# Kernel optimization log

Hardware: AMD Instinct MI355X
Metric: run time of the kernel (lower is better)

The kernel has to match this reference:

```python
import jax, jax.numpy as jnp
import numpy as np

DIM = 1024
HEADS = 16
DIM_HEAD = 64
INNER = HEADS * DIM_HEAD  # 1024
SCALE = DIM_HEAD ** -0.5


def setup_inputs() -> dict:
    key = jax.random.key(0)
    ks = jax.random.split(key, 7)
    b, n = 4, 1024
    x = jax.random.normal(ks[0], (b, n, DIM), dtype=jnp.float32)
    # Dense kernels (glorot-ish scale), mix-head matrices are N(0,1) as in source
    Wq = jax.random.normal(ks[1], (DIM, INNER), dtype=jnp.float32) * (DIM ** -0.5)
    Wkv = jax.random.normal(ks[2], (DIM, 2 * INNER), dtype=jnp.float32) * (DIM ** -0.5)
    mix_pre = jax.random.normal(ks[3], (HEADS, HEADS), dtype=jnp.float32)
    mix_post = jax.random.normal(ks[4], (HEADS, HEADS), dtype=jnp.float32)
    Wo = jax.random.normal(ks[5], (INNER, DIM), dtype=jnp.float32) * (INNER ** -0.5)
    bo = jnp.zeros((DIM,), dtype=jnp.float32)
    return {"x": x, "Wq": Wq, "Wkv": Wkv, "mix_pre": mix_pre,
            "mix_post": mix_post, "Wo": Wo, "bo": bo}


def reference(x, Wq, Wkv, mix_pre, mix_post, Wo, bo):
    b, n, _ = x.shape
    # context = x (self-attention path)
    q = x @ Wq                      # [b, n, inner]
    kv = x @ Wkv                    # [b, n, 2*inner]
    k, v = jnp.split(kv, 2, axis=-1)
    split_heads = lambda t: t.reshape(b, n, HEADS, DIM_HEAD).transpose(0, 2, 1, 3)
    q, k, v = map(split_heads, (q, k, v))  # [b, h, n, d]
    dots = jnp.einsum('bhid,bhjd->bhij', q, k) * SCALE
    dots = jnp.einsum('bhij,hg->bgij', dots, mix_pre)   # talking-heads pre-softmax
    attn = jax.nn.softmax(dots, axis=-1)
    attn = jnp.einsum('bhij,hg->bgij', attn, mix_post)  # talking-heads post-softmax
    out = jnp.einsum('bhij,bhjd->bhid', attn, v)        # [b, h, n, d]
    out = out.transpose(0, 2, 1, 3).reshape(b, n, INNER)
    return out @ Wo + bo            # dropout rate 0 -> identity
```

## Files before the change

### kernel.cpp

```cpp
#include <hip/hip_runtime.h>
#include <hip/hip_bf16.h>

using bf16 = __hip_bfloat16;

typedef __bf16 bf16x8 __attribute__((ext_vector_type(8)));
typedef __bf16 bf16x2v __attribute__((ext_vector_type(2)));
typedef float  f32x4  __attribute__((ext_vector_type(4)));
typedef float  f32x16 __attribute__((ext_vector_type(16)));

#define QK_SCALE 0.125f

__device__ __forceinline__ void load_lds16(const bf16* g, bf16* l) {
  __builtin_amdgcn_global_load_lds(
      (const __attribute__((address_space(1))) unsigned int*)g,
      (__attribute__((address_space(3))) unsigned int*)l, 16, 0, 0);
}

__device__ __forceinline__ unsigned pack_bf2(float a, float b) {
  bf16x2v v;
  v[0] = (__bf16)a;
  v[1] = (__bf16)b;
  return __builtin_bit_cast(unsigned, v);
}

struct alignas(8) bf16x4s { bf16 a, b, c, d; };
__global__ void f32_to_bf16_k(const float4* __restrict__ in, bf16x4s* __restrict__ out, int n4)
{
  const int i = blockIdx.x * blockDim.x + threadIdx.x;
  if (i < n4) {
    const float4 v = in[i];
    out[i] = { (bf16)v.x, (bf16)v.y, (bf16)v.z, (bf16)v.w };
  }
}

template<int TM, int TN, int WM, int WN, bool BIAS, typename CT>
__global__ __launch_bounds__(256, 2)
void gemm_nt(const bf16* __restrict__ A, const bf16* __restrict__ B,
             CT* __restrict__ C, const float* __restrict__ bias,
             int K, int lda, int ldb, int ldc,
             long sA0, long sA1, long sB0, long sB1, long sC0, long sC1,
             int nz1, float alpha)
{
  constexpr int BK = 32;
  constexpr int LDE = TN + 8;
  constexpr unsigned SB_STAGE = (TM + TN) * BK * 2;
  constexpr unsigned SB_EP = (sizeof(CT) == 2) ? TM * LDE * 2 : 0;
  constexpr unsigned SBYTES = SB_STAGE > SB_EP ? SB_STAGE : SB_EP;
  __shared__ __align__(16) char smem[SBYTES];
  bf16* lsA = (bf16*)smem;
  bf16* lsB = lsA + TM * BK;

  const int z = blockIdx.z;
  A += (long)(z / nz1) * sA0 + (long)(z % nz1) * sA1;
  B += (long)(z / nz1) * sB0 + (long)(z % nz1) * sB1;
  C += (long)(z / nz1) * sC0 + (long)(z % nz1) * sC1;
  const int tm0 = blockIdx.y * TM;
  const int tn0 = blockIdx.x * TN;

  const int tid = threadIdx.x;
  const int w = tid >> 6, l = tid & 63;
  constexpr int WCOLS = TN / WN;
  const int wm = (w / WCOLS) * WM, wn = (w % WCOLS) * WN;
  constexpr int AM = WM / 16, AN = WN / 16;
  f32x4 acc[AM][AN] = {};
  const int kg = l >> 4, rl = l & 15;

  constexpr int RA = TM / 64, RB = TN / 64;
  const int srow0 = tid >> 2;
  const int scol = tid & 3;

  for (int k0 = 0; k0 < K; k0 += BK) {
#pragma unroll
    for (int r = 0; r < RA; ++r) {
      const int row = r * 64 + srow0;
      const int col8 = scol ^ ((row >> 1) & 3);
      load_lds16(A + (long)(tm0 + row) * lda + (k0 + col8 * 8),
                 &lsA[row * BK + scol * 8]);
    }
#pragma unroll
    for (int r = 0; r < RB; ++r) {
      const int row = r * 64 + srow0;
      const int col8 = scol ^ ((row >> 1) & 3);
      load_lds16(B + (long)(tn0 + row) * ldb + (k0 + col8 * 8),
                 &lsB[row * BK + scol * 8]);
    }
    __syncthreads();

    bf16x8 af[AM], bfr[AN];
#pragma unroll
    for (int i = 0; i < AM; ++i) {
      const int m = wm + i * 16 + rl;
      const int p = kg ^ ((m >> 1) & 3);
      af[i] = *(const bf16x8*)&lsA[m * BK + p * 8];
    }
#pragma unroll
    for (int j = 0; j < AN; ++j) {
      const int n = wn + j * 16 + rl;
      const int p = kg ^ ((n >> 1) & 3);
      bfr[j] = *(const bf16x8*)&lsB[n * BK + p * 8];
    }
#pragma unroll
    for (int i = 0; i < AM; ++i)
#pragma unroll
      for (int j = 0; j < AN; ++j)
        acc[i][j] = __builtin_amdgcn_mfma_f32_16x16x32_bf16(af[i], bfr[j], acc[i][j], 0, 0, 0);
    __syncthreads();
  }

  if constexpr (sizeof(CT) == 2) {
    bf16* ep = (bf16*)smem;
#pragma unroll
    for (int i = 0; i < AM; ++i) {
#pragma unroll
      for (int j = 0; j < AN; ++j) {
        const int col = wn + j * 16 + rl;
        float bv = 0.f;
        if (BIAS) bv = bias[tn0 + col];
#pragma unroll
        for (int v = 0; v < 4; ++v) {
          const int row = wm + i * 16 + (l >> 4) * 4 + v;
          ep[row * LDE + col] = (bf16)(acc[i][j][v] * alpha + bv);
        }
      }
    }
    __syncthreads();
    constexpr int CH = (TM * TN) / 2048;
#pragma unroll
    for (int c = 0; c < CH; ++c) {
      const int gidx = (c * 256 + tid) * 8;
      const int row = gidx / TN, col = gidx % TN;
      *(uint4*)&C[(long)(tm0 + row) * ldc + tn0 + col] = *(const uint4*)&ep[row * LDE + col];
    }
  } else {
#pragma unroll
    for (int i = 0; i < AM; ++i) {
#pragma unroll
      for (int j = 0; j < AN; ++j) {
        const int col = tn0 + wn + j * 16 + rl;
        float bv = 0.f;
        if (BIAS) bv = bias[col];
#pragma unroll
        for (int v = 0; v < 4; ++v) {
          const int row = tm0 + wm + i * 16 + (l >> 4) * 4 + v;
          C[(long)row * ldc + col] = (CT)(acc[i][j][v] * alpha + bv);
        }
      }
    }
  }
}

template<typename TI>
__global__ void transpose_k(const TI* __restrict__ in, bf16* __restrict__ out,
                            int ldi, int ldo,
                            long sI0, long sI1, long sO0, long sO1, int nz1)
{
  __shared__ bf16 t[32][33];
  const int z = blockIdx.z;
  in  += (long)(z / nz1) * sI0 + (long)(z % nz1) * sI1;
  out += (long)(z / nz1) * sO0 + (long)(z % nz1) * sO1;
  const int c0 = blockIdx.x * 32, r0 = blockIdx.y * 32;
  const int x = threadIdx.x, y = threadIdx.y;
#pragma unroll
  for (int dy = 0; dy < 32; dy += 8)
    t[y + dy][x] = (bf16)(float)in[(long)(r0 + y + dy) * ldi + c0 + x];
  __syncthreads();
#pragma unroll
  for (int dy = 0; dy < 32; dy += 8)
    out[(long)(c0 + y + dy) * ldo + r0 + x] = t[x][y + dy];
}

__global__ __launch_bounds__(512, 1)
void mix_pv_fused(const bf16* __restrict__ S, const bf16* __restrict__ VTm,
                  bf16* __restrict__ O,
                  const float* __restrict__ mixpre, const float* __restrict__ mixpost)
{
  constexpr int SH = 1032;
  __shared__ __align__(16) __bf16 Sst[2][16 * SH];
  __shared__ __align__(16) __bf16 Pl[2][16 * 16 * 72];
  __shared__ float preS[256], postS[256];

  const int tid = threadIdx.x;
  const int l = tid & 63, w = tid >> 6;
  const int bx = blockIdx.x;
  const int b = bx & 3;
  const int i0 = (bx >> 2) << 4;

  if (tid < 256) preS[tid] = mixpre[tid];
  else           postS[tid - 256] = mixpost[tid - 256];
  __syncthreads();

  const int col = l & 31;
  const int H = l >> 5;
  const int g16 = l & 15;
  const bool loRow = (l & 16) != 0;
  const int rl16 = l & 15, kg4 = l >> 4;

  bf16x8 aPre, aPost;
#pragma unroll
  for (int e = 0; e < 8; ++e) {
    const int k = H * 8 + e;
    {
      const float c = preS[k * 16 + g16];
      const __bf16 hi = (__bf16)c;
      aPre[e] = loRow ? (__bf16)(c - (float)hi) : hi;
    }
    {
      const float c = postS[k * 16 + g16];
      const __bf16 hi = (__bf16)c;
      aPost[e] = loRow ? (__bf16)(c - (float)hi) : hi;
    }
  }

  const bf16* Sb = S + (long)b * 16777216 + (long)i0 * 1024;

  auto stage = [&](int t, int bufi) {
    const int jt = t * 64;
#pragma unroll
    for (int s = 0; s < 4; ++s) {
      const int h = 2 * w + (s >> 1);
      const int half = s & 1;
      const int i = half * 8 + (l >> 3);
      const int j = (l & 7) * 8;
      load_lds16(Sb + (long)h * 1048576 + (long)i * 1024 + jt + j,
                 (bf16*)&Sst[bufi][h * SH + half * 512 + l * 8]);
    }
  };

  float zac[2][8];
#pragma unroll
  for (int il = 0; il < 2; ++il)
#pragma unroll
    for (int k = 0; k < 8; ++k) zac[il][k] = 0.f;

  stage(0, 0);
  for (int t = 0; t < 16; ++t) {
    __syncthreads();
    if (t < 15) stage(t + 1, (t + 1) & 1);
    const __bf16* sb = Sst[t & 1];
#pragma unroll
    for (int il = 0; il < 2; ++il) {
      const int ic = 2 * w + il;
#pragma unroll
      for (int jh = 0; jh < 2; ++jh) {
        bf16x8 bfr;
#pragma unroll
        for (int e = 0; e < 8; ++e)
          bfr[e] = sb[(H * 8 + e) * SH + ic * 64 + jh * 32 + col];
        f32x16 d = {};
        d = __builtin_amdgcn_mfma_f32_32x32x16_bf16(aPre, bfr, d, 0, 0, 0);
#pragma unroll
        for (int k = 0; k < 8; ++k)
          zac[il][k] += __expf(d[k] + d[k + 8] - 10.f);
      }
    }
  }

#pragma unroll
  for (int il = 0; il < 2; ++il)
#pragma unroll
    for (int k = 0; k < 8; ++k) {
      float z = zac[il][k];
      z += __shfl_xor(z, 1, 64);
      z += __shfl_xor(z, 2, 64);
      z += __shfl_xor(z, 4, 64);
      z += __shfl_xor(z, 8, 64);
      z += __shfl_xor(z, 16, 64);
      zac[il][k] = 1.f / z;
    }

  f32x4 acc[2][4] = {};
  uint4 vreg[16];
  const bf16* vtg0 = VTm + ((long)(b * 16 + w) * 64) * 1024;
  const bf16* vtg1 = VTm + ((long)(b * 16 + w + 8) * 64) * 1024;

  stage(0, 0);
  for (int t = 0; t <= 16; ++t) {
    __syncthreads();

    if (t < 15) stage(t + 1, (t + 1) & 1);

    if (t > 0) {
      const __bf16* pb = Pl[(t - 1) & 1];
#pragma unroll
      for (int gi = 0; gi < 2; ++gi) {
        const int G = w + gi * 8;
#pragma unroll
        for (int kc = 0; kc < 2; ++kc) {
          const bf16x8 af = *(const bf16x8*)&pb[G * 1152 + rl16 * 72 + kc * 32 + kg4 * 8];
#pragma unroll
          for (int dt = 0; dt < 4; ++dt) {
            const bf16x8 bfv = __builtin_bit_cast(bf16x8, vreg[gi * 8 + kc * 4 + dt]);
            acc[gi][dt] = __builtin_amdgcn_mfma_f32_16x16x32_bf16(af, bfv, acc[gi][dt], 0, 0, 0);
          }
        }
      }
    }

    if (t < 16) {
      const int jt = t * 64;
#pragma unroll
      for (int kc = 0; kc < 2; ++kc)
#pragma unroll
        for (int dt = 0; dt < 4; ++dt) {
          vreg[kc * 4 + dt] =
              *(const uint4*)&vtg0[(long)(dt * 16 + rl16) * 1024 + jt + kc * 32 + kg4 * 8];
          vreg[8 + kc * 4 + dt] =
              *(const uint4*)&vtg1[(long)(dt * 16 + rl16) * 1024 + jt + kc * 32 + kg4 * 8];
        }

      const __bf16* sb = Sst[t & 1];
      __bf16* pl = Pl[t & 1];
#pragma unroll
      for (int il = 0; il < 2; ++il) {
        const int ic = 2 * w + il;
#pragma unroll
        for (int jh = 0; jh < 2; ++jh) {
          bf16x8 bfr;
#pragma unroll
          for (int e = 0; e < 8; ++e)
            bfr[e] = sb[(H * 8 + e) * SH + ic * 64 + jh * 32 + col];
          f32x16 d = {};
          d = __builtin_amdgcn_mfma_f32_32x32x16_bf16(aPre, bfr, d, 0, 0, 0);
          float pn[8];
#pragma unroll
          for (int k = 0; k < 8; ++k)
            pn[k] = __expf(d[k] + d[k + 8] - 10.f) * zac[il][k];
          const unsigned pA = pack_bf2(pn[0], pn[1]);
          const unsigned pB = pack_bf2(pn[2], pn[3]);
          const unsigned pC = pack_bf2(pn[4], pn[5]);
          const unsigned pD = pack_bf2(pn[6], pn[7]);
          const unsigned x0 = (unsigned)__shfl_xor((int)(H ? pA : pC), 32, 64);
          const unsigned x1 = (unsigned)__shfl_xor((int)(H ? pB : pD), 32, 64);
          uint4 praw;
          praw.x = H ? x0 : pA;
          praw.y = H ? x1 : pB;
          praw.z = H ? pC : x0;
          praw.w = H ? pD : x1;
          const bf16x8 pfr = __builtin_bit_cast(bf16x8, praw);
          f32x16 d2 = {};
          d2 = __builtin_amdgcn_mfma_f32_32x32x16_bf16(aPost, pfr, d2, 0, 0, 0);
#pragma unroll
          for (int k = 0; k < 8; ++k) {
            const int G = k + (k & 4) + (H << 2);
            pl[G * 1152 + ic * 72 + jh * 32 + col] = (__bf16)(d2[k] + d2[k + 8]);
          }
        }
      }
    }
  }

  const long ob = (long)(b * 1024 + i0) * 1024;
#pragma unroll
  for (int gi = 0; gi < 2; ++gi) {
    const int G = w + gi * 8;
#pragma unroll
    for (int dt = 0; dt < 4; ++dt)
#pragma unroll
      for (int v = 0; v < 4; ++v)
        O[ob + (long)((l >> 4) * 4 + v) * 1024 + G * 64 + dt * 16 + rl16] =
            (bf16)acc[gi][dt][v];
  }
}

extern "C" void kernel_launch(void* const* d_in, const int* in_sizes, int n_in,
                              void* d_out, int out_size, void* d_ws, size_t ws_size,
                              hipStream_t stream)
{
  const float* x     = (const float*)d_in[0];
  const float* Wq    = (const float*)d_in[1];
  const float* Wkv   = (const float*)d_in[2];
  const float* mpre  = (const float*)d_in[3];
  const float* mpost = (const float*)d_in[4];
  const float* Wo    = (const float*)d_in[5];
  const float* bo    = (const float*)d_in[6];
  float* out = (float*)d_out;

  char* ws = (char*)d_ws;
  const size_t MB = 1024 * 1024;
  if (ws_size < 184 * MB) return;
  bf16* xb   = (bf16*)(ws);
  bf16* QKV  = (bf16*)(ws + 8 * MB);
  bf16* WT   = (bf16*)(ws + 32 * MB);
  bf16* WoT  = (bf16*)(ws + 38 * MB);
  bf16* VT   = (bf16*)(ws + 40 * MB);
  bf16* Obuf = (bf16*)(ws + 48 * MB);
  bf16* Sbuf = (bf16*)(ws + 56 * MB);

  const dim3 tb(32, 8, 1);

  f32_to_bf16_k<<<4096, 256, 0, stream>>>((const float4*)x, (bf16x4s*)xb, 1048576);

  transpose_k<float><<<dim3(32, 32, 1), tb, 0, stream>>>(Wq,  WT,           1024, 1024, 0, 0, 0, 0, 1);
  transpose_k<float><<<dim3(64, 32, 1), tb, 0, stream>>>(Wkv, WT + 1048576, 2048, 1024, 0, 0, 0, 0, 1);
  transpose_k<float><<<dim3(32, 32, 1), tb, 0, stream>>>(Wo,  WoT,          1024, 1024, 0, 0, 0, 0, 1);

  gemm_nt<128, 128, 64, 64, false, bf16><<<dim3(24, 32, 1), 256, 0, stream>>>(
      xb, WT, QKV, nullptr, 1024, 1024, 1024, 3072, 0, 0, 0, 0, 0, 0, 1, 1.f);

  transpose_k<bf16><<<dim3(2, 32, 64), tb, 0, stream>>>(
      QKV + 2048, VT, 3072, 1024,
      3145728, 64, 16L * 65536, 65536, 16);

  gemm_nt<128, 128, 64, 64, false, bf16><<<dim3(8, 8, 64), 256, 0, stream>>>(
      QKV, QKV + 1024, Sbuf, nullptr, 64, 3072, 3072, 1024,
      3145728, 64, 3145728, 64, 16L * 1048576, 1048576, 16, QK_SCALE);

  mix_pv_fused<<<dim3(256, 1, 1), 512, 0, stream>>>(Sbuf, VT, Obuf, mpre, mpost);

  gemm_nt<128, 128, 64, 64, true, float><<<dim3(8, 32, 1), 256, 0, stream>>>(
      Obuf, WoT, out, bo, 1024, 1024, 1024, 1024, 0, 0, 0, 0, 0, 0, 1, 1.f);
}
```

Baseline: 291.7 us.

## Store scores head-interleaved and load them straight into registers in mix kernel

A new QK kernel writes the score tensor in a [b,i,j,head] layout, so each lane of the talking-heads mix kernel can fetch its 8-head MFMA operand with a single 16-byte global load. This replaces the LDS staging and the strided 8-element gathers from LDS. The softmax and PV loops now double-buffer score fragments in registers and use one lgkm-wait barrier per step, and the P tile stride is padded. The risks are a less efficient QK GEMM with scattered 8-byte stores, and higher register pressure in the fused kernel.

```diff
diff --git a/kernel.cpp b/kernel.cpp
--- a/kernel.cpp
+++ b/kernel.cpp
@@ -21,6 +21,10 @@
   v[0] = (__bf16)a;
   v[1] = (__bf16)b;
   return __builtin_bit_cast(unsigned, v);
+}
+
+__device__ __forceinline__ void barrier_lgkm() {
+  asm volatile("s_waitcnt lgkmcnt(0)\n\ts_barrier" ::: "memory");
 }
 
 struct alignas(8) bf16x4s { bf16 a, b, c, d; };
@@ -169,14 +173,48 @@
     out[(long)(c0 + y + dy) * ldo + r0 + x] = t[x][y + dy];
 }
 
+__global__ __launch_bounds__(256)
+void qk_int(const bf16* __restrict__ QKV, bf16* __restrict__ Sx)
+{
+  const int tid = threadIdx.x;
+  const int l = tid & 63, w = tid >> 6;
+  const int j0 = blockIdx.x * 32, i0 = blockIdx.y * 32, b = blockIdx.z;
+  const int row = l & 31, H = l >> 5;
+
+  const bf16* qb = QKV + (long)(b * 1024 + i0 + row) * 3072 + H * 8;
+  const bf16* kb = QKV + (long)(b * 1024 + j0 + row) * 3072 + 1024 + H * 8;
+  const int h0 = w * 4;
+
+  f32x16 acc[4] = {};
+#pragma unroll
+  for (int hh = 0; hh < 4; ++hh) {
+    const int hofs = (h0 + hh) * 64;
+#pragma unroll
+    for (int kc = 0; kc < 4; ++kc) {
+      const bf16x8 a  = *(const bf16x8*)(qb + hofs + kc * 16);
+      const bf16x8 bb = *(const bf16x8*)(kb + hofs + kc * 16);
+      acc[hh] = __builtin_amdgcn_mfma_f32_32x32x16_bf16(a, bb, acc[hh], 0, 0, 0);
+    }
+  }
+
+  bf16* sb = Sx + ((long)(b * 1024 + i0) * 1024 + j0) * 16 + h0;
+#pragma unroll
+  for (int k = 0; k < 16; ++k) {
+    const int irow = (k & 3) + 8 * (k >> 2) + 4 * H;
+    uint2 pv;
+    pv.x = pack_bf2(acc[0][k] * QK_SCALE, acc[1][k] * QK_SCALE);
+    pv.y = pack_bf2(acc[2][k] * QK_SCALE, acc[3][k] * QK_SCALE);
+    *(uint2*)(sb + (long)irow * 16384 + row * 16) = pv;
+  }
+}
+
 __global__ __launch_bounds__(512, 1)
 void mix_pv_fused(const bf16* __restrict__ S, const bf16* __restrict__ VTm,
                   bf16* __restrict__ O,
                   const float* __restrict__ mixpre, const float* __restrict__ mixpost)
 {
-  constexpr int SH = 1032;
-  __shared__ __align__(16) __bf16 Sst[2][16 * SH];
-  __shared__ __align__(16) __bf16 Pl[2][16 * 16 * 72];
+  constexpr int PLG = 1160;
+  __shared__ __align__(16) __bf16 Pl[2][16 * PLG];
   __shared__ float preS[256], postS[256];
 
   const int tid = threadIdx.x;
@@ -211,19 +249,21 @@
     }
   }
 
-  const bf16* Sb = S + (long)b * 16777216 + (long)i0 * 1024;
-
-  auto stage = [&](int t, int bufi) {
-    const int jt = t * 64;
-#pragma unroll
-    for (int s = 0; s < 4; ++s) {
-      const int h = 2 * w + (s >> 1);
-      const int half = s & 1;
-      const int i = half * 8 + (l >> 3);
-      const int j = (l & 7) * 8;
-      load_lds16(Sb + (long)h * 1048576 + (long)i * 1024 + jt + j,
-                 (bf16*)&Sst[bufi][h * SH + half * 512 + l * 8]);
-    }
+  const bf16* Sb = S + (long)(b * 1024 + i0) * 16384;
+  const bf16* sptr[2][2];
+#pragma unroll
+  for (int il = 0; il < 2; ++il)
+#pragma unroll
+    for (int jh = 0; jh < 2; ++jh)
+      sptr[il][jh] = Sb + (long)(2 * w + il) * 16384 + (jh * 32 + col) * 16 + H * 8;
+
+  auto loadS = [&](uint4* f, int t) {
+    const long to = (long)t * 1024;
+#pragma unroll
+    for (int il = 0; il < 2; ++il)
+#pragma unroll
+      for (int jh = 0; jh < 2; ++jh)
+        f[il * 2 + jh] = *(const uint4*)(sptr[il][jh] + to);
   };
 
   float zac[2][8];
@@ -232,27 +272,28 @@
 #pragma unroll
     for (int k = 0; k < 8; ++k) zac[il][k] = 0.f;
 
-  stage(0, 0);
-  for (int t = 0; t < 16; ++t) {
-    __syncthreads();
-    if (t < 15) stage(t + 1, (t + 1) & 1);
-    const __bf16* sb = Sst[t & 1];
-#pragma unroll
-    for (int il = 0; il < 2; ++il) {
-      const int ic = 2 * w + il;
+  auto mixZ = [&](const uint4* f) {
+#pragma unroll
+    for (int il = 0; il < 2; ++il)
 #pragma unroll
       for (int jh = 0; jh < 2; ++jh) {
-        bf16x8 bfr;
-#pragma unroll
-        for (int e = 0; e < 8; ++e)
-          bfr[e] = sb[(H * 8 + e) * SH + ic * 64 + jh * 32 + col];
+        const bf16x8 bfr = __builtin_bit_cast(bf16x8, f[il * 2 + jh]);
         f32x16 d = {};
         d = __builtin_amdgcn_mfma_f32_32x32x16_bf16(aPre, bfr, d, 0, 0, 0);
 #pragma unroll
         for (int k = 0; k < 8; ++k)
           zac[il][k] += __expf(d[k] + d[k + 8] - 10.f);
       }
-    }
+  };
+
+  uint4 sfA[4], sfB[4];
+
+  loadS(sfA, 0);
+  for (int tt = 0; tt < 16; tt += 2) {
+    loadS(sfB, tt + 1);
+    mixZ(sfA);
+    if (tt + 2 < 16) loadS(sfA, tt + 2);
+    mixZ(sfB);
   }
 
 #pragma unroll
@@ -273,20 +314,48 @@
   const bf16* vtg0 = VTm + ((long)(b * 16 + w) * 64) * 1024;
   const bf16* vtg1 = VTm + ((long)(b * 16 + w + 8) * 64) * 1024;
 
-  stage(0, 0);
-  for (int t = 0; t <= 16; ++t) {
-    __syncthreads();
-
-    if (t < 15) stage(t + 1, (t + 1) & 1);
-
+  auto body = [&](int t, uint4* fcur, uint4* fnext, __bf16* plw, const __bf16* plr) {
+    if (t + 1 < 16) loadS(fnext, t + 1);
+#pragma unroll
+    for (int il = 0; il < 2; ++il) {
+      const int ic = 2 * w + il;
+#pragma unroll
+      for (int jh = 0; jh < 2; ++jh) {
+        const bf16x8 bfr = __builtin_bit_cast(bf16x8, fcur[il * 2 + jh]);
+        f32x16 d = {};
+        d = __builtin_amdgcn_mfma_f32_32x32x16_bf16(aPre, bfr, d, 0, 0, 0);
+        float pn[8];
+#pragma unroll
+        for (int k = 0; k < 8; ++k)
+          pn[k] = __expf(d[k] + d[k + 8] - 10.f) * zac[il][k];
+        const unsigned pA = pack_bf2(pn[0], pn[1]);
+        const unsigned pB = pack_bf2(pn[2], pn[3]);
+        const unsigned pC = pack_bf2(pn[4], pn[5]);
+        const unsigned pD = pack_bf2(pn[6], pn[7]);
+        const unsigned x0 = (unsigned)__shfl_xor((int)(H ? pA : pC), 32, 64);
+        const unsigned x1 = (unsigned)__shfl_xor((int)(H ? pB : pD), 32, 64);
+        uint4 praw;
+        praw.x = H ? x0 : pA;
+        praw.y = H ? x1 : pB;
+        praw.z = H ? pC : x0;
+        praw.w = H ? pD : x1;
+        const bf16x8 pfr = __builtin_bit_cast(bf16x8, praw);
+        f32x16 d2 = {};
+        d2 = __builtin_amdgcn_mfma_f32_32x32x16_bf16(aPost, pfr, d2, 0, 0, 0);
+#pragma unroll
+        for (int k = 0; k < 8; ++k) {
+          const int G = k + (k & 4) + (H << 2);
+          plw[G * PLG + ic * 72 + jh * 32 + col] = (__bf16)(d2[k] + d2[k + 8]);
+        }
+      }
+    }
     if (t > 0) {
-      const __bf16* pb = Pl[(t - 1) & 1];
 #pragma unroll
       for (int gi = 0; gi < 2; ++gi) {
         const int G = w + gi * 8;
 #pragma unroll
         for (int kc = 0; kc < 2; ++kc) {
-          const bf16x8 af = *(const bf16x8*)&pb[G * 1152 + rl16 * 72 + kc * 32 + kg4 * 8];
+          const bf16x8 af = *(const bf16x8*)&plr[G * PLG + rl16 * 72 + kc * 32 + kg4 * 8];
 #pragma unroll
           for (int dt = 0; dt < 4; ++dt) {
             const bf16x8 bfv = __builtin_bit_cast(bf16x8, vreg[gi * 8 + kc * 4 + dt]);
@@ -295,8 +364,7 @@
         }
       }
     }
-
-    if (t < 16) {
+    {
       const int jt = t * 64;
 #pragma unroll
       for (int kc = 0; kc < 2; ++kc)
@@ -307,44 +375,26 @@
           vreg[8 + kc * 4 + dt] =
               *(const uint4*)&vtg1[(long)(dt * 16 + rl16) * 1024 + jt + kc * 32 + kg4 * 8];
         }
-
-      const __bf16* sb = Sst[t & 1];
-      __bf16* pl = Pl[t & 1];
-#pragma unroll
-      for (int il = 0; il < 2; ++il) {
-        const int ic = 2 * w + il;
-#pragma unroll
-        for (int jh = 0; jh < 2; ++jh) {
-          bf16x8 bfr;
-#pragma unroll
-          for (int e = 0; e < 8; ++e)
-            bfr[e] = sb[(H * 8 + e) * SH + ic * 64 + jh * 32 + col];
-          f32x16 d = {};
-          d = __builtin_amdgcn_mfma_f32_32x32x16_bf16(aPre, bfr, d, 0, 0, 0);
-          float pn[8];
-#pragma unroll
-          for (int k = 0; k < 8; ++k)
-            pn[k] = __expf(d[k] + d[k + 8] - 10.f) * zac[il][k];
-          const unsigned pA = pack_bf2(pn[0], pn[1]);
-          const unsigned pB = pack_bf2(pn[2], pn[3]);
-          const unsigned pC = pack_bf2(pn[4], pn[5]);
-          const unsigned pD = pack_bf2(pn[6], pn[7]);
-          const unsigned x0 = (unsigned)__shfl_xor((int)(H ? pA : pC), 32, 64);
-          const unsigned x1 = (unsigned)__shfl_xor((int)(H ? pB : pD), 32, 64);
-          uint4 praw;
-          praw.x = H ? x0 : pA;
-          praw.y = H ? x1 : pB;
-          praw.z = H ? pC : x0;
-          praw.w = H ? pD : x1;
-          const bf16x8 pfr = __builtin_bit_cast(bf16x8, praw);
-          f32x16 d2 = {};
-          d2 = __builtin_amdgcn_mfma_f32_32x32x16_bf16(aPost, pfr, d2, 0, 0, 0);
-#pragma unroll
-          for (int k = 0; k < 8; ++k) {
-            const int G = k + (k & 4) + (H << 2);
-            pl[G * 1152 + ic * 72 + jh * 32 + col] = (__bf16)(d2[k] + d2[k + 8]);
-          }
-        }
+    }
+    barrier_lgkm();
+  };
+
+  loadS(sfA, 0);
+  for (int tt = 0; tt < 16; tt += 2) {
+    body(tt,     sfA, sfB, Pl[0], Pl[1]);
+    body(tt + 1, sfB, sfA, Pl[1], Pl[0]);
+  }
+
+#pragma unroll
+  for (int gi = 0; gi < 2; ++gi) {
+    const int G = w + gi * 8;
+#pragma unroll
+    for (int kc = 0; kc < 2; ++kc) {
+      const bf16x8 af = *(const bf16x8*)&Pl[1][G * PLG + rl16 * 72 + kc * 32 + kg4 * 8];
+#pragma unroll
+      for (int dt = 0; dt < 4; ++dt) {
+        const bf16x8 bfv = __builtin_bit_cast(bf16x8, vreg[gi * 8 + kc * 4 + dt]);
+        acc[gi][dt] = __builtin_amdgcn_mfma_f32_16x16x32_bf16(af, bfv, acc[gi][dt], 0, 0, 0);
       }
     }
   }
@@ -401,9 +451,7 @@
       QKV + 2048, VT, 3072, 1024,
       3145728, 64, 16L * 65536, 65536, 16);
 
-  gemm_nt<128, 128, 64, 64, false, bf16><<<dim3(8, 8, 64), 256, 0, stream>>>(
-      QKV, QKV + 1024, Sbuf, nullptr, 64, 3072, 3072, 1024,
-      3145728, 64, 3145728, 64, 16L * 1048576, 1048576, 16, QK_SCALE);
+  qk_int<<<dim3(32, 32, 4), 256, 0, stream>>>(QKV, Sbuf);
 
   mix_pv_fused<<<dim3(256, 1, 1), 512, 0, stream>>>(Sbuf, VT, Obuf, mpre, mpost);
 
```

New measurement: 349.4 us. 19.8% more time.
